# Kernel optimization log

Measured on AMD Instinct MI355X. Metric: run time of the kernel, lower is better.

## Reference

```python
import jax, jax.numpy as jnp
import numpy as np

B, T, S, D = 8, 2048, 2048, 1024

def setup_inputs() -> dict:
    key = jax.random.key(0)
    k1, k2 = jax.random.split(key)
    trg_outs = jax.random.normal(k1, (B, T, D), dtype=jnp.float32)
    src_outs = jax.random.normal(k2, (B, S, D), dtype=jnp.float32)
    return {"trg_outs": trg_outs, "src_outs": src_outs}

def reference(trg_outs, src_outs):
    # Luong 'dot' attention: unscaled dot-product scores.
    # scores: (B, T, S)
    attn_scores = jnp.einsum('btd,bsd->bts', trg_outs, src_outs)
    attn_weights = jax.nn.softmax(attn_scores, axis=2)
    # context: (B, T, D)
    context_vec = jnp.einsum('bts,bsd->btd', attn_weights, src_outs)
    return (context_vec, attn_weights)
```

## Files before the change

### kernel.cpp

```cpp
#include <hip/hip_runtime.h>


#define BB 8
#define TT 2048
#define SS 2048
#define DD 1024

typedef float  f32x4   __attribute__((ext_vector_type(4)));
typedef float  f32x16  __attribute__((ext_vector_type(16)));
typedef short  bf16x8  __attribute__((ext_vector_type(8)));
typedef _Float16 f16x8 __attribute__((ext_vector_type(8)));
typedef _Float16 f16x4 __attribute__((ext_vector_type(4)));

static __device__ __forceinline__ unsigned short bf16_rne(float x) {
  unsigned int u = __float_as_uint(x);
  u += 0x7FFFu + ((u >> 16) & 1u);
  return (unsigned short)(u >> 16);
}

static __device__ __forceinline__ void gl2lds16(const void* g, void* l) {
  __builtin_amdgcn_global_load_lds(
      (const __attribute__((address_space(1))) unsigned int*)g,
      (__attribute__((address_space(3))) unsigned int*)l, 16, 0, 0);
}

__global__ __launch_bounds__(256)
void conv_trg_f16(const float* __restrict__ x, _Float16* __restrict__ h16) {
  const size_t i = ((size_t)blockIdx.x * 256 + threadIdx.x) * 8;
  float4 v0 = *(const float4*)(x + i);
  float4 v1 = *(const float4*)(x + i + 4);
  f16x8 h;
  h[0] = (_Float16)v0.x; h[1] = (_Float16)v0.y;
  h[2] = (_Float16)v0.z; h[3] = (_Float16)v0.w;
  h[4] = (_Float16)v1.x; h[5] = (_Float16)v1.y;
  h[6] = (_Float16)v1.z; h[7] = (_Float16)v1.w;
  *(f16x8*)(h16 + i) = h;
}

__global__ __launch_bounds__(256)
void conv_src_f16_hilo_t(const float* __restrict__ src,
                         _Float16* __restrict__ hi,
                         _Float16* __restrict__ lo,
                         _Float16* __restrict__ srcT) {
  const int b  = blockIdx.z;
  const int d0 = blockIdx.x * 64;
  const int s0 = blockIdx.y * 64;
  const float* S = src + (size_t)b * SS * DD;
  __shared__ _Float16 t16[64][65];
  const int t = threadIdx.x;

#pragma unroll
  for (int p = 0; p < 4; ++p) {
    const int r = p * 16 + (t >> 4);
    const int c = (t & 15) * 4;
    float4 v = *(const float4*)(S + (size_t)(s0 + r) * DD + d0 + c);
    float f[4] = {v.x, v.y, v.z, v.w};
    f16x4 h, l;
#pragma unroll
    for (int e = 0; e < 4; ++e) {
      _Float16 hv = (_Float16)f[e];
      h[e] = hv;
      l[e] = (_Float16)(f[e] - (float)hv);
      t16[r][c + e] = hv;
    }
    const size_t go = ((size_t)b * SS + s0 + r) * DD + d0 + c;
    *(f16x4*)(hi + go) = h;
    *(f16x4*)(lo + go) = l;
  }
  __syncthreads();
#pragma unroll
  for (int p = 0; p < 4; ++p) {
    const int d  = p * 16 + (t >> 4);
    const int sq = (t & 15) * 4;
    f16x4 o;
#pragma unroll
    for (int k = 0; k < 4; ++k) o[k] = t16[sq + k][d];
    *(f16x4*)(srcT + ((size_t)b * DD + d0 + d) * SS + s0 + sq) = o;
  }
}

__global__ __launch_bounds__(512, 2)
void attn_gemm1_pipe(const _Float16* __restrict__ a16,
                     const _Float16* __restrict__ bh16,
                     const _Float16* __restrict__ bl16,
                     float* __restrict__ scores) {
  const int b   = blockIdx.z;
  const int tm0 = blockIdx.y * 256;
  const int tn0 = blockIdx.x * 256;
  float* C = scores + (size_t)b * TT * SS;

  __shared__ __align__(16) _Float16 sm[3][3][8192];

  const int t      = threadIdx.x;
  const int lane   = t & 63;
  const int wv     = t >> 6;
  const int wm     = (wv >> 2) * 128;
  const int wn     = (wv & 3) * 64;
  const int lrow32 = lane & 31;
  const int khalf  = lane >> 5;

  const int s0 = t, s1 = t + 512;
  const int r0 = s0 >> 2, g0 = (s0 & 3) ^ ((r0 >> 1) & 3);
  const int r1 = s1 >> 2, g1 = (s1 & 3) ^ ((r1 >> 1) & 3);

  const _Float16* pA0  = a16  + ((size_t)b * TT + tm0 + r0) * DD + g0 * 8;
  const _Float16* pA1  = a16  + ((size_t)b * TT + tm0 + r1) * DD + g1 * 8;
  const _Float16* pBh0 = bh16 + ((size_t)b * SS + tn0 + r0) * DD + g0 * 8;
  const _Float16* pBh1 = bh16 + ((size_t)b * SS + tn0 + r1) * DD + g1 * 8;
  const _Float16* pBl0 = bl16 + ((size_t)b * SS + tn0 + r0) * DD + g0 * 8;
  const _Float16* pBl1 = bl16 + ((size_t)b * SS + tn0 + r1) * DD + g1 * 8;

#define STAGE1(dst)                                    \
  do {                                                 \
    gl2lds16(pA0,  (dst) + s0 * 8);                    \
    gl2lds16(pA1,  (dst) + s1 * 8);                    \
    gl2lds16(pBh0, (dst) + 8192 + s0 * 8);             \
    gl2lds16(pBh1, (dst) + 8192 + s1 * 8);             \
    gl2lds16(pBl0, (dst) + 16384 + s0 * 8);            \
    gl2lds16(pBl1, (dst) + 16384 + s1 * 8);            \
    pA0 += 32; pA1 += 32; pBh0 += 32; pBh1 += 32;      \
    pBl0 += 32; pBl1 += 32;                            \
  } while (0)

  f32x16 acc[4][2];
#pragma unroll
  for (int i = 0; i < 4; ++i)
#pragma unroll
    for (int j = 0; j < 2; ++j) acc[i][j] = (f32x16)0.0f;

  _Float16* bufc = &sm[0][0][0];
  _Float16* bufo = &sm[1][0][0];
  _Float16* bufn = &sm[2][0][0];

  STAGE1(bufc);
  STAGE1(bufo);
  asm volatile("s_waitcnt vmcnt(6)" ::: "memory");
  __builtin_amdgcn_s_barrier();
  __builtin_amdgcn_sched_barrier(0);

  const int NT = DD / 32;
#pragma unroll 1
  for (int tt = 0; tt < NT; ++tt) {
    if (tt + 2 < NT) STAGE1(bufn);

    const _Float16* As = bufc;
    const _Float16* Bh = bufc + 8192;
    const _Float16* Bl = bufc + 16384;
#pragma unroll
    for (int kk = 0; kk < 2; ++kk) {
      const int cb = kk * 2 + khalf;
      f16x8 a[4], bh[2], bl[2];
#pragma unroll
      for (int mi = 0; mi < 4; ++mi) {
        const int r = wm + mi * 32 + lrow32;
        a[mi] = *(const f16x8*)(As + (r * 4 + (cb ^ ((r >> 1) & 3))) * 8);
      }
#pragma unroll
      for (int ni = 0; ni < 2; ++ni) {
        const int r   = wn + ni * 32 + lrow32;
        const int off = (r * 4 + (cb ^ ((r >> 1) & 3))) * 8;
        bh[ni] = *(const f16x8*)(Bh + off);
        bl[ni] = *(const f16x8*)(Bl + off);
      }
      __builtin_amdgcn_s_setprio(1);
#pragma unroll
      for (int mi = 0; mi < 4; ++mi)
#pragma unroll
        for (int ni = 0; ni < 2; ++ni) {
          acc[mi][ni] = __builtin_amdgcn_mfma_f32_32x32x16_f16(a[mi], bh[ni], acc[mi][ni], 0, 0, 0);
          acc[mi][ni] = __builtin_amdgcn_mfma_f32_32x32x16_f16(a[mi], bl[ni], acc[mi][ni], 0, 0, 0);
        }
      __builtin_amdgcn_s_setprio(0);
    }

    if (tt + 2 < NT) asm volatile("s_waitcnt vmcnt(6)" ::: "memory");
    else             asm volatile("s_waitcnt vmcnt(0)" ::: "memory");
    __builtin_amdgcn_s_barrier();
    __builtin_amdgcn_sched_barrier(0);

    _Float16* tmp = bufc; bufc = bufo; bufo = bufn; bufn = tmp;
  }
#undef STAGE1

  const int rsub = 4 * khalf;
#pragma unroll
  for (int mi = 0; mi < 4; ++mi)
#pragma unroll
    for (int ni = 0; ni < 2; ++ni) {
      const int rb  = tm0 + wm + mi * 32 + rsub;
      const int col = tn0 + wn + ni * 32 + lrow32;
#pragma unroll
      for (int p = 0; p < 16; ++p)
        C[(size_t)(rb + (p & 3) + 8 * (p >> 2)) * SS + col] = acc[mi][ni][p];
    }
}

__global__ __launch_bounds__(64)
void attn_softmax_w16(float* __restrict__ w, _Float16* __restrict__ w16) {
  const size_t row = blockIdx.x;
  float4* p4 = (float4*)(w + row * SS);
  _Float16* o = w16 + row * SS;
  const int lane = threadIdx.x;

  float4 v[8];
#pragma unroll
  for (int j = 0; j < 8; ++j) v[j] = p4[lane + 64 * j];

  float m = -1e30f;
#pragma unroll
  for (int j = 0; j < 8; ++j)
    m = fmaxf(m, fmaxf(fmaxf(v[j].x, v[j].y), fmaxf(v[j].z, v[j].w)));
#pragma unroll
  for (int off = 32; off >= 1; off >>= 1) m = fmaxf(m, __shfl_xor(m, off, 64));

  float s = 0.0f;
#pragma unroll
  for (int j = 0; j < 8; ++j) {
    v[j].x = __expf(v[j].x - m); v[j].y = __expf(v[j].y - m);
    v[j].z = __expf(v[j].z - m); v[j].w = __expf(v[j].w - m);
    s += v[j].x + v[j].y + v[j].z + v[j].w;
  }
#pragma unroll
  for (int off = 32; off >= 1; off >>= 1) s += __shfl_xor(s, off, 64);

  const float inv = __fdividef(1.0f, s);
#pragma unroll
  for (int j = 0; j < 8; ++j) {
    v[j].x *= inv; v[j].y *= inv; v[j].z *= inv; v[j].w *= inv;
    p4[lane + 64 * j] = v[j];
    f16x4 h;
    h[0] = (_Float16)v[j].x; h[1] = (_Float16)v[j].y;
    h[2] = (_Float16)v[j].z; h[3] = (_Float16)v[j].w;
    *(f16x4*)(o + 4 * (lane + 64 * j)) = h;
  }
}

__global__ __launch_bounds__(512, 2)
void attn_gemm2_pipe(const _Float16* __restrict__ w16,
                     const _Float16* __restrict__ srcT,
                     float* __restrict__ out) {
  const int b   = blockIdx.z;
  const int tm0 = blockIdx.y * 256;
  const int tn0 = blockIdx.x * 256;
  float* C = out + (size_t)b * TT * DD;

  __shared__ __align__(16) _Float16 sm[3][2][8192];

  const int t      = threadIdx.x;
  const int lane   = t & 63;
  const int wv     = t >> 6;
  const int wm     = (wv >> 2) * 128;
  const int wn     = (wv & 3) * 64;
  const int lrow32 = lane & 31;
  const int khalf  = lane >> 5;

  const int s0 = t, s1 = t + 512;
  const int r0 = s0 >> 2, g0 = (s0 & 3) ^ ((r0 >> 1) & 3);
  const int r1 = s1 >> 2, g1 = (s1 & 3) ^ ((r1 >> 1) & 3);

  const _Float16* pA0 = w16  + ((size_t)b * TT + tm0 + r0) * SS + g0 * 8;
  const _Float16* pA1 = w16  + ((size_t)b * TT + tm0 + r1) * SS + g1 * 8;
  const _Float16* pB0 = srcT + ((size_t)b * DD + tn0 + r0) * SS + g0 * 8;
  const _Float16* pB1 = srcT + ((size_t)b * DD + tn0 + r1) * SS + g1 * 8;

#define STAGE2(dst)                                    \
  do {                                                 \
    gl2lds16(pA0, (dst) + s0 * 8);                     \
    gl2lds16(pA1, (dst) + s1 * 8);                     \
    gl2lds16(pB0, (dst) + 8192 + s0 * 8);              \
    gl2lds16(pB1, (dst) + 8192 + s1 * 8);              \
    pA0 += 32; pA1 += 32; pB0 += 32; pB1 += 32;        \
  } while (0)

  f32x16 acc[4][2];
#pragma unroll
  for (int i = 0; i < 4; ++i)
#pragma unroll
    for (int j = 0; j < 2; ++j) acc[i][j] = (f32x16)0.0f;

  _Float16* bufc = &sm[0][0][0];
  _Float16* bufo = &sm[1][0][0];
  _Float16* bufn = &sm[2][0][0];

  STAGE2(bufc);
  STAGE2(bufo);
  asm volatile("s_waitcnt vmcnt(4)" ::: "memory");
  __builtin_amdgcn_s_barrier();
  __builtin_amdgcn_sched_barrier(0);

  const int NT = SS / 32;
#pragma unroll 1
  for (int tt = 0; tt < NT; ++tt) {
    if (tt + 2 < NT) STAGE2(bufn);

    const _Float16* As = bufc;
    const _Float16* Bs = bufc + 8192;
#pragma unroll
    for (int kk = 0; kk < 2; ++kk) {
      const int cb = kk * 2 + khalf;
      f16x8 a[4], bf[2];
#pragma unroll
      for (int mi = 0; mi < 4; ++mi) {
        const int r = wm + mi * 32 + lrow32;
        a[mi] = *(const f16x8*)(As + (r * 4 + (cb ^ ((r >> 1) & 3))) * 8);
      }
#pragma unroll
      for (int ni = 0; ni < 2; ++ni) {
        const int r = wn + ni * 32 + lrow32;
        bf[ni] = *(const f16x8*)(Bs + (r * 4 + (cb ^ ((r >> 1) & 3))) * 8);
      }
      __builtin_amdgcn_s_setprio(1);
#pragma unroll
      for (int mi = 0; mi < 4; ++mi)
#pragma unroll
        for (int ni = 0; ni < 2; ++ni)
          acc[mi][ni] = __builtin_amdgcn_mfma_f32_32x32x16_f16(a[mi], bf[ni], acc[mi][ni], 0, 0, 0);
      __builtin_amdgcn_s_setprio(0);
    }

    if (tt + 2 < NT) asm volatile("s_waitcnt vmcnt(4)" ::: "memory");
    else             asm volatile("s_waitcnt vmcnt(0)" ::: "memory");
    __builtin_amdgcn_s_barrier();
    __builtin_amdgcn_sched_barrier(0);

    _Float16* tmp = bufc; bufc = bufo; bufo = bufn; bufn = tmp;
  }
#undef STAGE2

  const int rsub = 4 * khalf;
#pragma unroll
  for (int mi = 0; mi < 4; ++mi)
#pragma unroll
    for (int ni = 0; ni < 2; ++ni) {
      const int rb  = tm0 + wm + mi * 32 + rsub;
      const int col = tn0 + wn + ni * 32 + lrow32;
#pragma unroll
      for (int p = 0; p < 16; ++p)
        C[(size_t)(rb + (p & 3) + 8 * (p >> 2)) * DD + col] = acc[mi][ni][p];
    }
}

__global__ __launch_bounds__(256, 1)
void attn_gemm1_scores_bf16x3(const float* __restrict__ trg,
                              const float* __restrict__ src,
                              float* __restrict__ scores) {
  const int b   = blockIdx.z;
  const int tm0 = blockIdx.y * 128;
  const int tn0 = blockIdx.x * 128;
  const float* A  = trg + (size_t)b * TT * DD;
  const float* Bm = src + (size_t)b * SS * DD;
  float* C = scores + (size_t)b * TT * SS;

  __shared__ __align__(16) unsigned short smAh[128 * 32];
  __shared__ __align__(16) unsigned short smAl[128 * 32];
  __shared__ __align__(16) unsigned short smBh[128 * 32];
  __shared__ __align__(16) unsigned short smBl[128 * 32];

  const int t     = threadIdx.x;
  const int lane  = t & 63;
  const int wv    = t >> 6;
  const int m_off = (wv & 1) * 64;
  const int n_off = (wv >> 1) * 64;
  const int q     = lane >> 4;
  const int lrow  = lane & 15;

  f32x4 acc[4][4];
#pragma unroll
  for (int i = 0; i < 4; ++i)
#pragma unroll
    for (int j = 0; j < 4; ++j) acc[i][j] = (f32x4)0.0f;

  for (int kt = 0; kt < DD; kt += 32) {
    __syncthreads();
#pragma unroll
    for (int h = 0; h < 2; ++h) {
      const int c  = t + h * 256;
      const int r  = c >> 2;
      const int j  = c & 3;
      const int gk = j ^ ((r >> 1) & 3);
      {
        const float* ga = A + (size_t)(tm0 + r) * DD + kt + gk * 8;
        float4 v0 = *(const float4*)ga;
        float4 v1 = *(const float4*)(ga + 4);
        float f[8] = {v0.x, v0.y, v0.z, v0.w, v1.x, v1.y, v1.z, v1.w};
        bf16x8 hi, lo;
#pragma unroll
        for (int e = 0; e < 8; ++e) {
          unsigned short hb = bf16_rne(f[e]);
          hi[e] = (short)hb;
          float hf = __uint_as_float(((unsigned int)hb) << 16);
          lo[e] = (short)bf16_rne(f[e] - hf);
        }
        *(bf16x8*)(smAh + c * 8) = hi;
        *(bf16x8*)(smAl + c * 8) = lo;
      }
      {
        const float* gb = Bm + (size_t)(tn0 + r) * DD + kt + gk * 8;
        float4 v0 = *(const float4*)gb;
        float4 v1 = *(const float4*)(gb + 4);
        float f[8] = {v0.x, v0.y, v0.z, v0.w, v1.x, v1.y, v1.z, v1.w};
        bf16x8 hi, lo;
#pragma unroll
        for (int e = 0; e < 8; ++e) {
          unsigned short hb = bf16_rne(f[e]);
          hi[e] = (short)hb;
          float hf = __uint_as_float(((unsigned int)hb) << 16);
          lo[e] = (short)bf16_rne(f[e] - hf);
        }
        *(bf16x8*)(smBh + c * 8) = hi;
        *(bf16x8*)(smBl + c * 8) = lo;
      }
    }
    __syncthreads();

    bf16x8 ah[4], al[4], bh[4], bl[4];
#pragma unroll
    for (int mi = 0; mi < 4; ++mi) {
      const int r   = m_off + mi * 16 + lrow;
      const int off = (r * 4 + (q ^ ((r >> 1) & 3))) * 8;
      ah[mi] = *(const bf16x8*)(smAh + off);
      al[mi] = *(const bf16x8*)(smAl + off);
    }
#pragma unroll
    for (int ni = 0; ni < 4; ++ni) {
      const int r   = n_off + ni * 16 + lrow;
      const int off = (r * 4 + (q ^ ((r >> 1) & 3))) * 8;
      bh[ni] = *(const bf16x8*)(smBh + off);
      bl[ni] = *(const bf16x8*)(smBl + off);
    }
#pragma unroll
    for (int mi = 0; mi < 4; ++mi)
#pragma unroll
      for (int ni = 0; ni < 4; ++ni) {
        acc[mi][ni] = __builtin_amdgcn_mfma_f32_16x16x32_bf16(al[mi], bh[ni], acc[mi][ni], 0, 0, 0);
        acc[mi][ni] = __builtin_amdgcn_mfma_f32_16x16x32_bf16(ah[mi], bl[ni], acc[mi][ni], 0, 0, 0);
        acc[mi][ni] = __builtin_amdgcn_mfma_f32_16x16x32_bf16(ah[mi], bh[ni], acc[mi][ni], 0, 0, 0);
      }
  }

#pragma unroll
  for (int mi = 0; mi < 4; ++mi)
#pragma unroll
    for (int ni = 0; ni < 4; ++ni) {
      const int row0 = tm0 + m_off + mi * 16 + q * 4;
      const int col  = tn0 + n_off + ni * 16 + lrow;
#pragma unroll
      for (int p = 0; p < 4; ++p)
        C[(size_t)(row0 + p) * SS + col] = acc[mi][ni][p];
    }
}

__global__ __launch_bounds__(256)
void attn_softmax_rows(float* __restrict__ w) {
  float* p = w + (size_t)blockIdx.x * SS;
  const int t = threadIdx.x;
  float4* p4 = (float4*)p;
  float4 v0 = p4[t];
  float4 v1 = p4[t + 256];

  float m = fmaxf(fmaxf(fmaxf(v0.x, v0.y), fmaxf(v0.z, v0.w)),
                  fmaxf(fmaxf(v1.x, v1.y), fmaxf(v1.z, v1.w)));
#pragma unroll
  for (int off = 32; off >= 1; off >>= 1) m = fmaxf(m, __shfl_xor(m, off, 64));
  __shared__ float redm[4];
  __shared__ float reds[4];
  const int wv = t >> 6, lane = t & 63;
  if (lane == 0) redm[wv] = m;
  __syncthreads();
  m = fmaxf(fmaxf(redm[0], redm[1]), fmaxf(redm[2], redm[3]));

  v0.x = __expf(v0.x - m); v0.y = __expf(v0.y - m);
  v0.z = __expf(v0.z - m); v0.w = __expf(v0.w - m);
  v1.x = __expf(v1.x - m); v1.y = __expf(v1.y - m);
  v1.z = __expf(v1.z - m); v1.w = __expf(v1.w - m);

  float s = v0.x + v0.y + v0.z + v0.w + v1.x + v1.y + v1.z + v1.w;
#pragma unroll
  for (int off = 32; off >= 1; off >>= 1) s += __shfl_xor(s, off, 64);
  if (lane == 0) reds[wv] = s;
  __syncthreads();
  s = reds[0] + reds[1] + reds[2] + reds[3];

  const float inv = __fdividef(1.0f, s);
  v0.x *= inv; v0.y *= inv; v0.z *= inv; v0.w *= inv;
  v1.x *= inv; v1.y *= inv; v1.z *= inv; v1.w *= inv;
  p4[t] = v0;
  p4[t + 256] = v1;
}

__global__ __launch_bounds__(256, 1)
void attn_gemm2_ctx_f16(const float* __restrict__ w,
                        const float* __restrict__ src,
                        float* __restrict__ out) {
  const int b   = blockIdx.z;
  const int tm0 = blockIdx.y * 128;
  const int tn0 = blockIdx.x * 128;
  const float* A  = w + (size_t)b * TT * SS;
  const float* Bs = src + (size_t)b * SS * DD;
  float* C = out + (size_t)b * TT * DD;

  __shared__ __align__(16) _Float16 smA[128 * 32];
  __shared__ __align__(16) _Float16 smB[128 * 32];

  const int t     = threadIdx.x;
  const int lane  = t & 63;
  const int wv    = t >> 6;
  const int m_off = (wv & 1) * 64;
  const int n_off = (wv >> 1) * 64;
  const int q     = lane >> 4;
  const int lrow  = lane & 15;

  const int bn    = t & 127;
  const int bh2   = t >> 7;
  const int bs2   = (bn >> 1) & 3;
  const int slot0 = (2 * bh2) ^ bs2;
  const int slot1 = (2 * bh2 + 1) ^ bs2;

  f32x4 acc[4][4];
#pragma unroll
  for (int i = 0; i < 4; ++i)
#pragma unroll
    for (int j = 0; j < 4; ++j) acc[i][j] = (f32x4)0.0f;

  for (int kt = 0; kt < SS; kt += 32) {
    __syncthreads();
#pragma unroll
    for (int h = 0; h < 2; ++h) {
      const int c  = t + h * 256;
      const int r  = c >> 2;
      const int j  = c & 3;
      const int gk = j ^ ((r >> 1) & 3);
      const float* ga = A + (size_t)(tm0 + r) * SS + kt + gk * 8;
      float4 v0 = *(const float4*)ga;
      float4 v1 = *(const float4*)(ga + 4);
      f16x8 hv;
      hv[0] = (_Float16)v0.x; hv[1] = (_Float16)v0.y;
      hv[2] = (_Float16)v0.z; hv[3] = (_Float16)v0.w;
      hv[4] = (_Float16)v1.x; hv[5] = (_Float16)v1.y;
      hv[6] = (_Float16)v1.z; hv[7] = (_Float16)v1.w;
      *(f16x8*)(smA + c * 8) = hv;
    }
    {
      const float* gb = Bs + (size_t)(kt + bh2 * 16) * DD + (tn0 + bn);
      f16x8 c0, c1;
#pragma unroll
      for (int kk = 0; kk < 8; ++kk) c0[kk] = (_Float16)gb[(size_t)kk * DD];
#pragma unroll
      for (int kk = 0; kk < 8; ++kk) c1[kk] = (_Float16)gb[(size_t)(kk + 8) * DD];
      *(f16x8*)(smB + bn * 32 + slot0 * 8) = c0;
      *(f16x8*)(smB + bn * 32 + slot1 * 8) = c1;
    }
    __syncthreads();

    f16x8 af[4], bfr[4];
#pragma unroll
    for (int mi = 0; mi < 4; ++mi) {
      const int r   = m_off + mi * 16 + lrow;
      const int off = (r * 4 + (q ^ ((r >> 1) & 3))) * 8;
      af[mi] = *(const f16x8*)(smA + off);
    }
#pragma unroll
    for (int ni = 0; ni < 4; ++ni) {
      const int n   = n_off + ni * 16 + lrow;
      const int off = n * 32 + (q ^ ((n >> 1) & 3)) * 8;
      bfr[ni] = *(const f16x8*)(smB + off);
    }
#pragma unroll
    for (int mi = 0; mi < 4; ++mi)
#pragma unroll
      for (int ni = 0; ni < 4; ++ni)
        acc[mi][ni] = __builtin_amdgcn_mfma_f32_16x16x32_f16(af[mi], bfr[ni], acc[mi][ni], 0, 0, 0);
  }

#pragma unroll
  for (int mi = 0; mi < 4; ++mi)
#pragma unroll
    for (int ni = 0; ni < 4; ++ni) {
      const int row0 = tm0 + m_off + mi * 16 + q * 4;
      const int col  = tn0 + n_off + ni * 16 + lrow;
#pragma unroll
      for (int p = 0; p < 4; ++p)
        C[(size_t)(row0 + p) * DD + col] = acc[mi][ni][p];
    }
}

extern "C" void kernel_launch(void* const* d_in, const int* in_sizes, int n_in,
                              void* d_out, int out_size, void* d_ws, size_t ws_size,
                              hipStream_t stream) {
  const float* trg = (const float*)d_in[0];
  const float* src = (const float*)d_in[1];
  float* ctx = (float*)d_out;
  float* wts = (float*)d_out + (size_t)BB * TT * DD;

  const size_t NT = (size_t)BB * TT * DD;
  const size_t NW = (size_t)BB * TT * SS;
  const size_t need = (4 * NT + NW) * 2;

  if (ws_size >= need) {
    _Float16* tH16 = (_Float16*)d_ws;
    _Float16* sH16 = tH16 + NT;
    _Float16* sL16 = sH16 + NT;
    _Float16* srcT = sL16 + NT;
    _Float16* w16  = srcT + NT;

    conv_trg_f16<<<dim3(NT / (8 * 256)), 256, 0, stream>>>(trg, tH16);
    conv_src_f16_hilo_t<<<dim3(DD / 64, SS / 64, BB), 256, 0, stream>>>(src, sH16, sL16, srcT);
    attn_gemm1_pipe<<<dim3(SS / 256, TT / 256, BB), 512, 0, stream>>>(tH16, sH16, sL16, wts);
    attn_softmax_w16<<<dim3(BB * TT), 64, 0, stream>>>(wts, w16);
    attn_gemm2_pipe<<<dim3(DD / 256, TT / 256, BB), 512, 0, stream>>>(w16, srcT, ctx);
  } else {
    attn_gemm1_scores_bf16x3<<<dim3(SS / 128, TT / 128, BB), 256, 0, stream>>>(trg, src, wts);
    attn_softmax_rows<<<dim3(BB * TT), 256, 0, stream>>>(wts);
    attn_gemm2_ctx_f16<<<dim3(DD / 128, TT / 128, BB), 256, 0, stream>>>(wts, src, ctx);
  }
}
```

Baseline: 558.6 us.

## Split K-tile into halves with interleaved async loads and barrier ping-pong in GEMMs

Both pipelined GEMM kernels now store each K-tile in LDS as two 16-wide halves, using a new swizzle (ldsoff_h) with LDS offsets computed once outside the loop. Each iteration issues half of the next stage's global-to-LDS loads between the LDS reads and the MFMA block of each half, with extra barriers around the MFMA sections. The goal is to spread memory traffic across the compute phases, reduce per-iteration address arithmetic, and lower LDS bank conflicts. In exchange each iteration has several more barriers, which can stall waves.

```diff
diff --git a/kernel.cpp b/kernel.cpp
--- a/kernel.cpp
+++ b/kernel.cpp
@@ -22,6 +22,10 @@
   __builtin_amdgcn_global_load_lds(
       (const __attribute__((address_space(1))) unsigned int*)g,
       (__attribute__((address_space(3))) unsigned int*)l, 16, 0, 0);
+}
+
+static __device__ __forceinline__ int ldsoff_h(int r, int h) {
+  return ((r >> 2) << 6) + ((((r & 3) << 1) + (h ^ ((r >> 2) & 1))) << 3);
 }
 
 __global__ __launch_bounds__(256)
@@ -89,7 +93,7 @@
   const int tn0 = blockIdx.x * 256;
   float* C = scores + (size_t)b * TT * SS;
 
-  __shared__ __align__(16) _Float16 sm[3][3][8192];
+  __shared__ __align__(16) _Float16 sm[3][24576];
 
   const int t      = threadIdx.x;
   const int lane   = t & 63;
@@ -99,28 +103,34 @@
   const int lrow32 = lane & 31;
   const int khalf  = lane >> 5;
 
-  const int s0 = t, s1 = t + 512;
-  const int r0 = s0 >> 2, g0 = (s0 & 3) ^ ((r0 >> 1) & 3);
-  const int r1 = s1 >> 2, g1 = (s1 & 3) ^ ((r1 >> 1) & 3);
-
-  const _Float16* pA0  = a16  + ((size_t)b * TT + tm0 + r0) * DD + g0 * 8;
-  const _Float16* pA1  = a16  + ((size_t)b * TT + tm0 + r1) * DD + g1 * 8;
-  const _Float16* pBh0 = bh16 + ((size_t)b * SS + tn0 + r0) * DD + g0 * 8;
-  const _Float16* pBh1 = bh16 + ((size_t)b * SS + tn0 + r1) * DD + g1 * 8;
-  const _Float16* pBl0 = bl16 + ((size_t)b * SS + tn0 + r0) * DD + g0 * 8;
-  const _Float16* pBl1 = bl16 + ((size_t)b * SS + tn0 + r1) * DD + g1 * 8;
-
-#define STAGE1(dst)                                    \
-  do {                                                 \
-    gl2lds16(pA0,  (dst) + s0 * 8);                    \
-    gl2lds16(pA1,  (dst) + s1 * 8);                    \
-    gl2lds16(pBh0, (dst) + 8192 + s0 * 8);             \
-    gl2lds16(pBh1, (dst) + 8192 + s1 * 8);             \
-    gl2lds16(pBl0, (dst) + 16384 + s0 * 8);            \
-    gl2lds16(pBl1, (dst) + 16384 + s1 * 8);            \
-    pA0 += 32; pA1 += 32; pBh0 += 32; pBh1 += 32;      \
-    pBl0 += 32; pBl1 += 32;                            \
-  } while (0)
+  const _Float16* gp[6];
+  {
+    const _Float16* base0 = a16  + ((size_t)b * TT + tm0) * DD;
+    const _Float16* base1 = bh16 + ((size_t)b * SS + tn0) * DD;
+    const _Float16* base2 = bl16 + ((size_t)b * SS + tn0) * DD;
+    const _Float16* bases[3] = {base0, base1, base2};
+#pragma unroll
+    for (int j = 0; j < 6; ++j) {
+      const int kk   = j & 1;
+      const int cc   = t;
+      const int line = cc >> 3, slot = cc & 7;
+      const int r    = (line << 2) + (slot >> 1);
+      const int h    = (slot & 1) ^ (line & 1);
+      gp[j] = bases[j >> 1] + (size_t)r * DD + kk * 16 + h * 8;
+    }
+  }
+#define STG1(buf, j) do { gl2lds16(gp[j], (buf) + ((j) * 512 + t) * 8); gp[j] += 32; } while (0)
+
+  int aoff[4], bhoff[2], bloff[2];
+#pragma unroll
+  for (int mi = 0; mi < 4; ++mi)
+    aoff[mi] = ldsoff_h(wm + mi * 32 + lrow32, khalf);
+#pragma unroll
+  for (int ni = 0; ni < 2; ++ni) {
+    const int rr = wn + ni * 32 + lrow32;
+    bhoff[ni] = 8192  + ldsoff_h(rr, khalf);
+    bloff[ni] = 16384 + ldsoff_h(rr, khalf);
+  }
 
   f32x16 acc[4][2];
 #pragma unroll
@@ -128,12 +138,14 @@
 #pragma unroll
     for (int j = 0; j < 2; ++j) acc[i][j] = (f32x16)0.0f;
 
-  _Float16* bufc = &sm[0][0][0];
-  _Float16* bufo = &sm[1][0][0];
-  _Float16* bufn = &sm[2][0][0];
-
-  STAGE1(bufc);
-  STAGE1(bufo);
+  _Float16* bufc = sm[0];
+  _Float16* bufo = sm[1];
+  _Float16* bufn = sm[2];
+
+#pragma unroll
+  for (int j = 0; j < 6; ++j) STG1(bufc, j);
+#pragma unroll
+  for (int j = 0; j < 6; ++j) STG1(bufo, j);
   asm volatile("s_waitcnt vmcnt(6)" ::: "memory");
   __builtin_amdgcn_s_barrier();
   __builtin_amdgcn_sched_barrier(0);
@@ -141,27 +153,21 @@
   const int NT = DD / 32;
 #pragma unroll 1
   for (int tt = 0; tt < NT; ++tt) {
-    if (tt + 2 < NT) STAGE1(bufn);
-
-    const _Float16* As = bufc;
-    const _Float16* Bh = bufc + 8192;
-    const _Float16* Bl = bufc + 16384;
-#pragma unroll
-    for (int kk = 0; kk < 2; ++kk) {
-      const int cb = kk * 2 + khalf;
+    const bool more = (tt + 2 < NT);
+
+    {
       f16x8 a[4], bh[2], bl[2];
 #pragma unroll
-      for (int mi = 0; mi < 4; ++mi) {
-        const int r = wm + mi * 32 + lrow32;
-        a[mi] = *(const f16x8*)(As + (r * 4 + (cb ^ ((r >> 1) & 3))) * 8);
+      for (int mi = 0; mi < 4; ++mi) a[mi] = *(const f16x8*)(bufc + aoff[mi]);
+#pragma unroll
+      for (int ni = 0; ni < 2; ++ni) {
+        bh[ni] = *(const f16x8*)(bufc + bhoff[ni]);
+        bl[ni] = *(const f16x8*)(bufc + bloff[ni]);
       }
-#pragma unroll
-      for (int ni = 0; ni < 2; ++ni) {
-        const int r   = wn + ni * 32 + lrow32;
-        const int off = (r * 4 + (cb ^ ((r >> 1) & 3))) * 8;
-        bh[ni] = *(const f16x8*)(Bh + off);
-        bl[ni] = *(const f16x8*)(Bl + off);
-      }
+      if (more) { STG1(bufn, 0); STG1(bufn, 1); STG1(bufn, 2); }
+      __builtin_amdgcn_s_barrier();
+      asm volatile("s_waitcnt lgkmcnt(0)" ::: "memory");
+      __builtin_amdgcn_sched_barrier(0);
       __builtin_amdgcn_s_setprio(1);
 #pragma unroll
       for (int mi = 0; mi < 4; ++mi)
@@ -171,16 +177,41 @@
           acc[mi][ni] = __builtin_amdgcn_mfma_f32_32x32x16_f16(a[mi], bl[ni], acc[mi][ni], 0, 0, 0);
         }
       __builtin_amdgcn_s_setprio(0);
-    }
-
-    if (tt + 2 < NT) asm volatile("s_waitcnt vmcnt(6)" ::: "memory");
-    else             asm volatile("s_waitcnt vmcnt(0)" ::: "memory");
-    __builtin_amdgcn_s_barrier();
-    __builtin_amdgcn_sched_barrier(0);
+      __builtin_amdgcn_s_barrier();
+      __builtin_amdgcn_sched_barrier(0);
+    }
+
+    {
+      f16x8 a[4], bh[2], bl[2];
+#pragma unroll
+      for (int mi = 0; mi < 4; ++mi) a[mi] = *(const f16x8*)(bufc + 4096 + aoff[mi]);
+#pragma unroll
+      for (int ni = 0; ni < 2; ++ni) {
+        bh[ni] = *(const f16x8*)(bufc + 4096 + bhoff[ni]);
+        bl[ni] = *(const f16x8*)(bufc + 4096 + bloff[ni]);
+      }
+      if (more) { STG1(bufn, 3); STG1(bufn, 4); STG1(bufn, 5); }
+      if (more) asm volatile("s_waitcnt vmcnt(6)" ::: "memory");
+      else      asm volatile("s_waitcnt vmcnt(0)" ::: "memory");
+      __builtin_amdgcn_s_barrier();
+      asm volatile("s_waitcnt lgkmcnt(0)" ::: "memory");
+      __builtin_amdgcn_sched_barrier(0);
+      __builtin_amdgcn_s_setprio(1);
+#pragma unroll
+      for (int mi = 0; mi < 4; ++mi)
+#pragma unroll
+        for (int ni = 0; ni < 2; ++ni) {
+          acc[mi][ni] = __builtin_amdgcn_mfma_f32_32x32x16_f16(a[mi], bh[ni], acc[mi][ni], 0, 0, 0);
+          acc[mi][ni] = __builtin_amdgcn_mfma_f32_32x32x16_f16(a[mi], bl[ni], acc[mi][ni], 0, 0, 0);
+        }
+      __builtin_amdgcn_s_setprio(0);
+      __builtin_amdgcn_s_barrier();
+      __builtin_amdgcn_sched_barrier(0);
+    }
 
     _Float16* tmp = bufc; bufc = bufo; bufo = bufn; bufn = tmp;
   }
-#undef STAGE1
+#undef STG1
 
   const int rsub = 4 * khalf;
 #pragma unroll
@@ -244,7 +275,7 @@
   const int tn0 = blockIdx.x * 256;
   float* C = out + (size_t)b * TT * DD;
 
-  __shared__ __align__(16) _Float16 sm[3][2][8192];
+  __shared__ __align__(16) _Float16 sm[3][16384];
 
   const int t      = threadIdx.x;
   const int lane   = t & 63;
@@ -254,23 +285,30 @@
   const int lrow32 = lane & 31;
   const int khalf  = lane >> 5;
 
-  const int s0 = t, s1 = t + 512;
-  const int r0 = s0 >> 2, g0 = (s0 & 3) ^ ((r0 >> 1) & 3);
-  const int r1 = s1 >> 2, g1 = (s1 & 3) ^ ((r1 >> 1) & 3);
-
-  const _Float16* pA0 = w16  + ((size_t)b * TT + tm0 + r0) * SS + g0 * 8;
-  const _Float16* pA1 = w16  + ((size_t)b * TT + tm0 + r1) * SS + g1 * 8;
-  const _Float16* pB0 = srcT + ((size_t)b * DD + tn0 + r0) * SS + g0 * 8;
-  const _Float16* pB1 = srcT + ((size_t)b * DD + tn0 + r1) * SS + g1 * 8;
-
-#define STAGE2(dst)                                    \
-  do {                                                 \
-    gl2lds16(pA0, (dst) + s0 * 8);                     \
-    gl2lds16(pA1, (dst) + s1 * 8);                     \
-    gl2lds16(pB0, (dst) + 8192 + s0 * 8);              \
-    gl2lds16(pB1, (dst) + 8192 + s1 * 8);              \
-    pA0 += 32; pA1 += 32; pB0 += 32; pB1 += 32;        \
-  } while (0)
+  const _Float16* gp[4];
+  {
+    const _Float16* base0 = w16  + ((size_t)b * TT + tm0) * SS;
+    const _Float16* base1 = srcT + ((size_t)b * DD + tn0) * SS;
+    const _Float16* bases[2] = {base0, base1};
+#pragma unroll
+    for (int j = 0; j < 4; ++j) {
+      const int kk   = j & 1;
+      const int cc   = t;
+      const int line = cc >> 3, slot = cc & 7;
+      const int r    = (line << 2) + (slot >> 1);
+      const int h    = (slot & 1) ^ (line & 1);
+      gp[j] = bases[j >> 1] + (size_t)r * SS + kk * 16 + h * 8;
+    }
+  }
+#define STG2(buf, j) do { gl2lds16(gp[j], (buf) + ((j) * 512 + t) * 8); gp[j] += 32; } while (0)
+
+  int aoff[4], boff[2];
+#pragma unroll
+  for (int mi = 0; mi < 4; ++mi)
+    aoff[mi] = ldsoff_h(wm + mi * 32 + lrow32, khalf);
+#pragma unroll
+  for (int ni = 0; ni < 2; ++ni)
+    boff[ni] = 8192 + ldsoff_h(wn + ni * 32 + lrow32, khalf);
 
   f32x16 acc[4][2];
 #pragma unroll
@@ -278,12 +316,14 @@
 #pragma unroll
     for (int j = 0; j < 2; ++j) acc[i][j] = (f32x16)0.0f;
 
-  _Float16* bufc = &sm[0][0][0];
-  _Float16* bufo = &sm[1][0][0];
-  _Float16* bufn = &sm[2][0][0];
-
-  STAGE2(bufc);
-  STAGE2(bufo);
+  _Float16* bufc = sm[0];
+  _Float16* bufo = sm[1];
+  _Float16* bufn = sm[2];
+
+#pragma unroll
+  for (int j = 0; j < 4; ++j) STG2(bufc, j);
+#pragma unroll
+  for (int j = 0; j < 4; ++j) STG2(bufo, j);
   asm volatile("s_waitcnt vmcnt(4)" ::: "memory");
   __builtin_amdgcn_s_barrier();
   __builtin_amdgcn_sched_barrier(0);
@@ -291,24 +331,18 @@
   const int NT = SS / 32;
 #pragma unroll 1
   for (int tt = 0; tt < NT; ++tt) {
-    if (tt + 2 < NT) STAGE2(bufn);
-
-    const _Float16* As = bufc;
-    const _Float16* Bs = bufc + 8192;
-#pragma unroll
-    for (int kk = 0; kk < 2; ++kk) {
-      const int cb = kk * 2 + khalf;
+    const bool more = (tt + 2 < NT);
+
+    {
       f16x8 a[4], bf[2];
 #pragma unroll
-      for (int mi = 0; mi < 4; ++mi) {
-        const int r = wm + mi * 32 + lrow32;
-        a[mi] = *(const f16x8*)(As + (r * 4 + (cb ^ ((r >> 1) & 3))) * 8);
-      }
-#pragma unroll
-      for (int ni = 0; ni < 2; ++ni) {
-        const int r = wn + ni * 32 + lrow32;
-        bf[ni] = *(const f16x8*)(Bs + (r * 4 + (cb ^ ((r >> 1) & 3))) * 8);
-      }
+      for (int mi = 0; mi < 4; ++mi) a[mi] = *(const f16x8*)(bufc + aoff[mi]);
+#pragma unroll
+      for (int ni = 0; ni < 2; ++ni) bf[ni] = *(const f16x8*)(bufc + boff[ni]);
+      if (more) { STG2(bufn, 0); STG2(bufn, 2); }
+      __builtin_amdgcn_s_barrier();
+      asm volatile("s_waitcnt lgkmcnt(0)" ::: "memory");
+      __builtin_amdgcn_sched_barrier(0);
       __builtin_amdgcn_s_setprio(1);
 #pragma unroll
       for (int mi = 0; mi < 4; ++mi)
@@ -316,16 +350,36 @@
         for (int ni = 0; ni < 2; ++ni)
           acc[mi][ni] = __builtin_amdgcn_mfma_f32_32x32x16_f16(a[mi], bf[ni], acc[mi][ni], 0, 0, 0);
       __builtin_amdgcn_s_setprio(0);
-    }
-
-    if (tt + 2 < NT) asm volatile("s_waitcnt vmcnt(4)" ::: "memory");
-    else             asm volatile("s_waitcnt vmcnt(0)" ::: "memory");
-    __builtin_amdgcn_s_barrier();
-    __builtin_amdgcn_sched_barrier(0);
+      __builtin_amdgcn_s_barrier();
+      __builtin_amdgcn_sched_barrier(0);
+    }
+
+    {
+      f16x8 a[4], bf[2];
+#pragma unroll
+      for (int mi = 0; mi < 4; ++mi) a[mi] = *(const f16x8*)(bufc + 4096 + aoff[mi]);
+#pragma unroll
+      for (int ni = 0; ni < 2; ++ni) bf[ni] = *(const f16x8*)(bufc + 4096 + boff[ni]);
+      if (more) { STG2(bufn, 1); STG2(bufn, 3); }
+      if (more) asm volatile("s_waitcnt vmcnt(4)" ::: "memory");
+      else      asm volatile("s_waitcnt vmcnt(0)" ::: "memory");
+      __builtin_amdgcn_s_barrier();
+      asm volatile("s_waitcnt lgkmcnt(0)" ::: "memory");
+      __builtin_amdgcn_sched_barrier(0);
+      __builtin_amdgcn_s_setprio(1);
+#pragma unroll
+      for (int mi = 0; mi < 4; ++mi)
+#pragma unroll
+        for (int ni = 0; ni < 2; ++ni)
+          acc[mi][ni] = __builtin_amdgcn_mfma_f32_32x32x16_f16(a[mi], bf[ni], acc[mi][ni], 0, 0, 0);
+      __builtin_amdgcn_s_setprio(0);
+      __builtin_amdgcn_s_barrier();
+      __builtin_amdgcn_sched_barrier(0);
+    }
 
     _Float16* tmp = bufc; bufc = bufo; bufo = bufn; bufn = tmp;
   }
-#undef STAGE2
+#undef STG2
 
   const int rsub = 4 * khalf;
 #pragma unroll
```

After: 575.5 us. 1.03x slower.

## Pre-swizzle B operands into MFMA fragment layout and load directly to registers

Applied to the files above, without the earlier changes.

The source conversion kernel now writes the hi/lo f16 split and the transposed copy in a fragment-major layout matching the MFMA 32x32x16 B operand. Both GEMMs then load B fragments straight from global memory into registers, double-buffered across half-k phases, and stage only the A tile through LDS with a new swizzle. This cuts LDS footprint and LDS traffic and removes the B LDS reads. The cost is more global loads per wave (B is no longer shared across waves in the block via LDS), an extra barrier per phase, and hand-tuned vmcnt counts that must match the load order exactly.

```diff
diff --git a/kernel.cpp b/kernel.cpp
--- a/kernel.cpp
+++ b/kernel.cpp
@@ -22,6 +22,10 @@
   __builtin_amdgcn_global_load_lds(
       (const __attribute__((address_space(1))) unsigned int*)g,
       (__attribute__((address_space(3))) unsigned int*)l, 16, 0, 0);
+}
+
+static __device__ __forceinline__ int ldsoff_h(int r, int h) {
+  return ((r >> 2) << 6) + ((((r & 3) << 1) + (h ^ ((r >> 2) & 1))) << 3);
 }
 
 __global__ __launch_bounds__(256)
@@ -38,10 +42,10 @@
 }
 
 __global__ __launch_bounds__(256)
-void conv_src_f16_hilo_t(const float* __restrict__ src,
-                         _Float16* __restrict__ hi,
-                         _Float16* __restrict__ lo,
-                         _Float16* __restrict__ srcT) {
+void conv_src_frag(const float* __restrict__ src,
+                   _Float16* __restrict__ bhp,
+                   _Float16* __restrict__ blp,
+                   _Float16* __restrict__ tp) {
   const int b  = blockIdx.z;
   const int d0 = blockIdx.x * 64;
   const int s0 = blockIdx.y * 64;
@@ -50,46 +54,58 @@
   const int t = threadIdx.x;
 
 #pragma unroll
-  for (int p = 0; p < 4; ++p) {
-    const int r = p * 16 + (t >> 4);
-    const int c = (t & 15) * 4;
-    float4 v = *(const float4*)(S + (size_t)(s0 + r) * DD + d0 + c);
-    float f[4] = {v.x, v.y, v.z, v.w};
-    f16x4 h, l;
-#pragma unroll
-    for (int e = 0; e < 4; ++e) {
+  for (int p = 0; p < 2; ++p) {
+    const int idx  = p * 256 + t;
+    const int dgrp = idx & 7;
+    const int srow = idx >> 3;
+    const float* g = S + (size_t)(s0 + srow) * DD + d0 + dgrp * 8;
+    float4 v0 = *(const float4*)g;
+    float4 v1 = *(const float4*)(g + 4);
+    float f[8] = {v0.x, v0.y, v0.z, v0.w, v1.x, v1.y, v1.z, v1.w};
+    f16x8 h, l;
+#pragma unroll
+    for (int e = 0; e < 8; ++e) {
       _Float16 hv = (_Float16)f[e];
       h[e] = hv;
       l[e] = (_Float16)(f[e] - (float)hv);
-      t16[r][c + e] = hv;
-    }
-    const size_t go = ((size_t)b * SS + s0 + r) * DD + d0 + c;
-    *(f16x4*)(hi + go) = h;
-    *(f16x4*)(lo + go) = l;
+      t16[srow][dgrp * 8 + e] = hv;
+    }
+    const int d   = d0 + dgrp * 8;
+    const int s   = s0 + srow;
+    const size_t base = ((size_t)b * 64 + (d >> 4)) * 32768 +
+                        (size_t)(s >> 5) * 512 +
+                        (size_t)((((d >> 3) & 1) * 32 + (s & 31)) * 8);
+    *(f16x8*)(bhp + base) = h;
+    *(f16x8*)(blp + base) = l;
   }
   __syncthreads();
 #pragma unroll
-  for (int p = 0; p < 4; ++p) {
-    const int d  = p * 16 + (t >> 4);
-    const int sq = (t & 15) * 4;
-    f16x4 o;
-#pragma unroll
-    for (int k = 0; k < 4; ++k) o[k] = t16[sq + k][d];
-    *(f16x4*)(srcT + ((size_t)b * DD + d0 + d) * SS + s0 + sq) = o;
+  for (int p = 0; p < 2; ++p) {
+    const int d64  = t & 63;
+    const int sgrp = p * 4 + (t >> 6);
+    f16x8 o;
+#pragma unroll
+    for (int k = 0; k < 8; ++k) o[k] = t16[sgrp * 8 + k][d64];
+    const int d = d0 + d64;
+    const int s = s0 + sgrp * 8;
+    const size_t base = ((size_t)b * 128 + (s >> 4)) * 16384 +
+                        (size_t)(d >> 5) * 512 +
+                        (size_t)((((s >> 3) & 1) * 32 + (d & 31)) * 8);
+    *(f16x8*)(tp + base) = o;
   }
 }
 
 __global__ __launch_bounds__(512, 2)
 void attn_gemm1_pipe(const _Float16* __restrict__ a16,
-                     const _Float16* __restrict__ bh16,
-                     const _Float16* __restrict__ bl16,
+                     const _Float16* __restrict__ bhp,
+                     const _Float16* __restrict__ blp,
                      float* __restrict__ scores) {
   const int b   = blockIdx.z;
   const int tm0 = blockIdx.y * 256;
   const int tn0 = blockIdx.x * 256;
   float* C = scores + (size_t)b * TT * SS;
 
-  __shared__ __align__(16) _Float16 sm[3][3][8192];
+  __shared__ __align__(16) _Float16 sm[3][8192];
 
   const int t      = threadIdx.x;
   const int lane   = t & 63;
@@ -99,88 +115,96 @@
   const int lrow32 = lane & 31;
   const int khalf  = lane >> 5;
 
-  const int s0 = t, s1 = t + 512;
-  const int r0 = s0 >> 2, g0 = (s0 & 3) ^ ((r0 >> 1) & 3);
-  const int r1 = s1 >> 2, g1 = (s1 & 3) ^ ((r1 >> 1) & 3);
-
-  const _Float16* pA0  = a16  + ((size_t)b * TT + tm0 + r0) * DD + g0 * 8;
-  const _Float16* pA1  = a16  + ((size_t)b * TT + tm0 + r1) * DD + g1 * 8;
-  const _Float16* pBh0 = bh16 + ((size_t)b * SS + tn0 + r0) * DD + g0 * 8;
-  const _Float16* pBh1 = bh16 + ((size_t)b * SS + tn0 + r1) * DD + g1 * 8;
-  const _Float16* pBl0 = bl16 + ((size_t)b * SS + tn0 + r0) * DD + g0 * 8;
-  const _Float16* pBl1 = bl16 + ((size_t)b * SS + tn0 + r1) * DD + g1 * 8;
-
-#define STAGE1(dst)                                    \
-  do {                                                 \
-    gl2lds16(pA0,  (dst) + s0 * 8);                    \
-    gl2lds16(pA1,  (dst) + s1 * 8);                    \
-    gl2lds16(pBh0, (dst) + 8192 + s0 * 8);             \
-    gl2lds16(pBh1, (dst) + 8192 + s1 * 8);             \
-    gl2lds16(pBl0, (dst) + 16384 + s0 * 8);            \
-    gl2lds16(pBl1, (dst) + 16384 + s1 * 8);            \
-    pA0 += 32; pA1 += 32; pBh0 += 32; pBh1 += 32;      \
-    pBl0 += 32; pBl1 += 32;                            \
+  const int ar = (t >> 3) * 4 + ((t & 7) >> 1);
+  const int ah = ((t & 7) & 1) ^ ((t >> 3) & 1);
+  const _Float16* gpA0 = a16 + ((size_t)b * TT + tm0 + ar) * DD + ah * 8;
+  const _Float16* gpA1 = gpA0 + 16;
+
+  const _Float16* bh_base = bhp + (size_t)b * 2097152 +
+                            (size_t)((tn0 + wn) >> 5) * 512 + (size_t)lane * 8;
+  const _Float16* bl_base = blp + (size_t)b * 2097152 +
+                            (size_t)((tn0 + wn) >> 5) * 512 + (size_t)lane * 8;
+
+  int aoff[4];
+#pragma unroll
+  for (int mi = 0; mi < 4; ++mi)
+    aoff[mi] = ldsoff_h(wm + mi * 32 + lrow32, khalf);
+
+  f32x16 acc[4][2];
+#pragma unroll
+  for (int i = 0; i < 4; ++i)
+#pragma unroll
+    for (int j = 0; j < 2; ++j) acc[i][j] = (f32x16)0.0f;
+
+  f16x8 bhA[2], blA[2], bhB[2], blB[2];
+
+  _Float16* bufc = sm[0];
+  _Float16* bufo = sm[1];
+  _Float16* bufn = sm[2];
+
+#define G1_LOADB(QQ, BH, BL)                                                \
+  do {                                                                      \
+    BH[0] = *(const f16x8*)(bh_base + (size_t)(QQ) * 32768);                \
+    BH[1] = *(const f16x8*)(bh_base + (size_t)(QQ) * 32768 + 512);          \
+    BL[0] = *(const f16x8*)(bl_base + (size_t)(QQ) * 32768);                \
+    BL[1] = *(const f16x8*)(bl_base + (size_t)(QQ) * 32768 + 512);          \
   } while (0)
 
-  f32x16 acc[4][2];
-#pragma unroll
-  for (int i = 0; i < 4; ++i)
-#pragma unroll
-    for (int j = 0; j < 2; ++j) acc[i][j] = (f32x16)0.0f;
-
-  _Float16* bufc = &sm[0][0][0];
-  _Float16* bufo = &sm[1][0][0];
-  _Float16* bufn = &sm[2][0][0];
-
-  STAGE1(bufc);
-  STAGE1(bufo);
-  asm volatile("s_waitcnt vmcnt(6)" ::: "memory");
+#define G1_PHASE(AOFFADD, DOLOADB, QN, BHN, BLN, DOSTAGE, AJ, VM, BHC, BLC) \
+  {                                                                         \
+    f16x8 af[4];                                                            \
+    _Pragma("unroll") for (int mi = 0; mi < 4; ++mi)                        \
+      af[mi] = *(const f16x8*)(bufc + (AOFFADD) + aoff[mi]);                \
+    asm volatile("" ::: "memory");                                          \
+    if (DOLOADB) { G1_LOADB(QN, BHN, BLN); }                                \
+    asm volatile("" ::: "memory");                                          \
+    if (DOSTAGE) {                                                          \
+      gl2lds16((AJ) ? (const void*)gpA1 : (const void*)gpA0,                \
+               bufn + (AJ) * 4096 + t * 8);                                 \
+    }                                                                       \
+    asm volatile("s_waitcnt vmcnt(" #VM ")" ::: "memory");                  \
+    __builtin_amdgcn_s_barrier();                                           \
+    asm volatile("s_waitcnt lgkmcnt(0)" ::: "memory");                      \
+    __builtin_amdgcn_sched_barrier(0);                                      \
+    __builtin_amdgcn_s_setprio(1);                                          \
+    _Pragma("unroll") for (int mi = 0; mi < 4; ++mi)                        \
+      _Pragma("unroll") for (int ni = 0; ni < 2; ++ni) {                    \
+        acc[mi][ni] = __builtin_amdgcn_mfma_f32_32x32x16_f16(af[mi], BHC[ni], acc[mi][ni], 0, 0, 0); \
+        acc[mi][ni] = __builtin_amdgcn_mfma_f32_32x32x16_f16(af[mi], BLC[ni], acc[mi][ni], 0, 0, 0); \
+      }                                                                     \
+    __builtin_amdgcn_s_setprio(0);                                          \
+    __builtin_amdgcn_s_barrier();                                           \
+    __builtin_amdgcn_sched_barrier(0);                                      \
+  }
+
+  gl2lds16(gpA0, sm[0] + t * 8);
+  gl2lds16(gpA1, sm[0] + 4096 + t * 8);
+  gpA0 += 32; gpA1 += 32;
+  asm volatile("" ::: "memory");
+  G1_LOADB(0, bhA, blA);
+  asm volatile("" ::: "memory");
+  gl2lds16(gpA0, sm[1] + t * 8);
+  gl2lds16(gpA1, sm[1] + 4096 + t * 8);
+  gpA0 += 32; gpA1 += 32;
+  asm volatile("s_waitcnt vmcnt(2)" ::: "memory");
   __builtin_amdgcn_s_barrier();
   __builtin_amdgcn_sched_barrier(0);
 
-  const int NT = DD / 32;
 #pragma unroll 1
-  for (int tt = 0; tt < NT; ++tt) {
-    if (tt + 2 < NT) STAGE1(bufn);
-
-    const _Float16* As = bufc;
-    const _Float16* Bh = bufc + 8192;
-    const _Float16* Bl = bufc + 16384;
-#pragma unroll
-    for (int kk = 0; kk < 2; ++kk) {
-      const int cb = kk * 2 + khalf;
-      f16x8 a[4], bh[2], bl[2];
-#pragma unroll
-      for (int mi = 0; mi < 4; ++mi) {
-        const int r = wm + mi * 32 + lrow32;
-        a[mi] = *(const f16x8*)(As + (r * 4 + (cb ^ ((r >> 1) & 3))) * 8);
-      }
-#pragma unroll
-      for (int ni = 0; ni < 2; ++ni) {
-        const int r   = wn + ni * 32 + lrow32;
-        const int off = (r * 4 + (cb ^ ((r >> 1) & 3))) * 8;
-        bh[ni] = *(const f16x8*)(Bh + off);
-        bl[ni] = *(const f16x8*)(Bl + off);
-      }
-      __builtin_amdgcn_s_setprio(1);
-#pragma unroll
-      for (int mi = 0; mi < 4; ++mi)
-#pragma unroll
-        for (int ni = 0; ni < 2; ++ni) {
-          acc[mi][ni] = __builtin_amdgcn_mfma_f32_32x32x16_f16(a[mi], bh[ni], acc[mi][ni], 0, 0, 0);
-          acc[mi][ni] = __builtin_amdgcn_mfma_f32_32x32x16_f16(a[mi], bl[ni], acc[mi][ni], 0, 0, 0);
-        }
-      __builtin_amdgcn_s_setprio(0);
-    }
-
-    if (tt + 2 < NT) asm volatile("s_waitcnt vmcnt(6)" ::: "memory");
-    else             asm volatile("s_waitcnt vmcnt(0)" ::: "memory");
-    __builtin_amdgcn_s_barrier();
-    __builtin_amdgcn_sched_barrier(0);
-
+  for (int tt = 0; tt < 30; ++tt) {
+    G1_PHASE(0,    1, 2 * tt + 1, bhB, blB, 1, 0, 6, bhA, blA);
+    G1_PHASE(4096, 1, 2 * tt + 2, bhA, blA, 1, 1, 6, bhB, blB);
+    gpA0 += 32; gpA1 += 32;
     _Float16* tmp = bufc; bufc = bufo; bufo = bufn; bufn = tmp;
   }
-#undef STAGE1
+  G1_PHASE(0,    1, 61, bhB, blB, 0, 0, 5, bhA, blA);
+  G1_PHASE(4096, 1, 62, bhA, blA, 0, 1, 4, bhB, blB);
+  { _Float16* tmp = bufc; bufc = bufo; bufo = bufn; bufn = tmp; }
+  G1_PHASE(0,    1, 63, bhB, blB, 0, 0, 4, bhA, blA);
+  G1_PHASE(4096, 0, 0,  bhA, blA, 0, 1, 0, bhB, blB);
+
+#undef G1_PHASE
+#undef G1_LOADB
 
   const int rsub = 4 * khalf;
 #pragma unroll
@@ -237,14 +261,14 @@
 
 __global__ __launch_bounds__(512, 2)
 void attn_gemm2_pipe(const _Float16* __restrict__ w16,
-                     const _Float16* __restrict__ srcT,
+                     const _Float16* __restrict__ tp,
                      float* __restrict__ out) {
   const int b   = blockIdx.z;
   const int tm0 = blockIdx.y * 256;
   const int tn0 = blockIdx.x * 256;
   float* C = out + (size_t)b * TT * DD;
 
-  __shared__ __align__(16) _Float16 sm[3][2][8192];
+  __shared__ __align__(16) _Float16 sm[3][8192];
 
   const int t      = threadIdx.x;
   const int lane   = t & 63;
@@ -254,78 +278,90 @@
   const int lrow32 = lane & 31;
   const int khalf  = lane >> 5;
 
-  const int s0 = t, s1 = t + 512;
-  const int r0 = s0 >> 2, g0 = (s0 & 3) ^ ((r0 >> 1) & 3);
-  const int r1 = s1 >> 2, g1 = (s1 & 3) ^ ((r1 >> 1) & 3);
-
-  const _Float16* pA0 = w16  + ((size_t)b * TT + tm0 + r0) * SS + g0 * 8;
-  const _Float16* pA1 = w16  + ((size_t)b * TT + tm0 + r1) * SS + g1 * 8;
-  const _Float16* pB0 = srcT + ((size_t)b * DD + tn0 + r0) * SS + g0 * 8;
-  const _Float16* pB1 = srcT + ((size_t)b * DD + tn0 + r1) * SS + g1 * 8;
-
-#define STAGE2(dst)                                    \
-  do {                                                 \
-    gl2lds16(pA0, (dst) + s0 * 8);                     \
-    gl2lds16(pA1, (dst) + s1 * 8);                     \
-    gl2lds16(pB0, (dst) + 8192 + s0 * 8);              \
-    gl2lds16(pB1, (dst) + 8192 + s1 * 8);              \
-    pA0 += 32; pA1 += 32; pB0 += 32; pB1 += 32;        \
+  const int ar = (t >> 3) * 4 + ((t & 7) >> 1);
+  const int ah = ((t & 7) & 1) ^ ((t >> 3) & 1);
+  const _Float16* gpA0 = w16 + ((size_t)b * TT + tm0 + ar) * SS + ah * 8;
+  const _Float16* gpA1 = gpA0 + 16;
+
+  const _Float16* tb_base = tp + (size_t)b * 2097152 +
+                            (size_t)((tn0 + wn) >> 5) * 512 + (size_t)lane * 8;
+
+  int aoff[4];
+#pragma unroll
+  for (int mi = 0; mi < 4; ++mi)
+    aoff[mi] = ldsoff_h(wm + mi * 32 + lrow32, khalf);
+
+  f32x16 acc[4][2];
+#pragma unroll
+  for (int i = 0; i < 4; ++i)
+#pragma unroll
+    for (int j = 0; j < 2; ++j) acc[i][j] = (f32x16)0.0f;
+
+  f16x8 bfA[2], bfB[2];
+
+  _Float16* bufc = sm[0];
+  _Float16* bufo = sm[1];
+  _Float16* bufn = sm[2];
+
+#define G2_LOADB(QQ, BF)                                                    \
+  do {                                                                      \
+    BF[0] = *(const f16x8*)(tb_base + (size_t)(QQ) * 16384);                \
+    BF[1] = *(const f16x8*)(tb_base + (size_t)(QQ) * 16384 + 512);          \
   } while (0)
 
-  f32x16 acc[4][2];
-#pragma unroll
-  for (int i = 0; i < 4; ++i)
-#pragma unroll
-    for (int j = 0; j < 2; ++j) acc[i][j] = (f32x16)0.0f;
-
-  _Float16* bufc = &sm[0][0][0];
-  _Float16* bufo = &sm[1][0][0];
-  _Float16* bufn = &sm[2][0][0];
-
-  STAGE2(bufc);
-  STAGE2(bufo);
-  asm volatile("s_waitcnt vmcnt(4)" ::: "memory");
+#define G2_PHASE(AOFFADD, DOLOADB, QN, BFN, DOSTAGE, AJ, VM, BFC)           \
+  {                                                                         \
+    f16x8 af[4];                                                            \
+    _Pragma("unroll") for (int mi = 0; mi < 4; ++mi)                        \
+      af[mi] = *(const f16x8*)(bufc + (AOFFADD) + aoff[mi]);                \
+    asm volatile("" ::: "memory");                                          \
+    if (DOLOADB) { G2_LOADB(QN, BFN); }                                     \
+    asm volatile("" ::: "memory");                                          \
+    if (DOSTAGE) {                                                          \
+      gl2lds16((AJ) ? (const void*)gpA1 : (const void*)gpA0,                \
+               bufn + (AJ) * 4096 + t * 8);                                 \
+    }                                                                       \
+    asm volatile("s_waitcnt vmcnt(" #VM ")" ::: "memory");                  \
+    __builtin_amdgcn_s_barrier();                                           \
+    asm volatile("s_waitcnt lgkmcnt(0)" ::: "memory");                      \
+    __builtin_amdgcn_sched_barrier(0);                                      \
+    __builtin_amdgcn_s_setprio(1);                                          \
+    _Pragma("unroll") for (int mi = 0; mi < 4; ++mi)                        \
+      _Pragma("unroll") for (int ni = 0; ni < 2; ++ni)                      \
+        acc[mi][ni] = __builtin_amdgcn_mfma_f32_32x32x16_f16(af[mi], BFC[ni], acc[mi][ni], 0, 0, 0); \
+    __builtin_amdgcn_s_setprio(0);                                          \
+    __builtin_amdgcn_s_barrier();                                           \
+    __builtin_amdgcn_sched_barrier(0);                                      \
+  }
+
+  gl2lds16(gpA0, sm[0] + t * 8);
+  gl2lds16(gpA1, sm[0] + 4096 + t * 8);
+  gpA0 += 32; gpA1 += 32;
+  asm volatile("" ::: "memory");
+  G2_LOADB(0, bfA);
+  asm volatile("" ::: "memory");
+  gl2lds16(gpA0, sm[1] + t * 8);
+  gl2lds16(gpA1, sm[1] + 4096 + t * 8);
+  gpA0 += 32; gpA1 += 32;
+  asm volatile("s_waitcnt vmcnt(2)" ::: "memory");
   __builtin_amdgcn_s_barrier();
   __builtin_amdgcn_sched_barrier(0);
 
-  const int NT = SS / 32;
 #pragma unroll 1
-  for (int tt = 0; tt < NT; ++tt) {
-    if (tt + 2 < NT) STAGE2(bufn);
-
-    const _Float16* As = bufc;
-    const _Float16* Bs = bufc + 8192;
-#pragma unroll
-    for (int kk = 0; kk < 2; ++kk) {
-      const int cb = kk * 2 + khalf;
-      f16x8 a[4], bf[2];
-#pragma unroll
-      for (int mi = 0; mi < 4; ++mi) {
-        const int r = wm + mi * 32 + lrow32;
-        a[mi] = *(const f16x8*)(As + (r * 4 + (cb ^ ((r >> 1) & 3))) * 8);
-      }
-#pragma unroll
-      for (int ni = 0; ni < 2; ++ni) {
-        const int r = wn + ni * 32 + lrow32;
-        bf[ni] = *(const f16x8*)(Bs + (r * 4 + (cb ^ ((r >> 1) & 3))) * 8);
-      }
-      __builtin_amdgcn_s_setprio(1);
-#pragma unroll
-      for (int mi = 0; mi < 4; ++mi)
-#pragma unroll
-        for (int ni = 0; ni < 2; ++ni)
-          acc[mi][ni] = __builtin_amdgcn_mfma_f32_32x32x16_f16(a[mi], bf[ni], acc[mi][ni], 0, 0, 0);
-      __builtin_amdgcn_s_setprio(0);
-    }
-
-    if (tt + 2 < NT) asm volatile("s_waitcnt vmcnt(4)" ::: "memory");
-    else             asm volatile("s_waitcnt vmcnt(0)" ::: "memory");
-    __builtin_amdgcn_s_barrier();
-    __builtin_amdgcn_sched_barrier(0);
-
+  for (int tt = 0; tt < 62; ++tt) {
+    G2_PHASE(0,    1, 2 * tt + 1, bfB, 1, 0, 4, bfA);
+    G2_PHASE(4096, 1, 2 * tt + 2, bfA, 1, 1, 4, bfB);
+    gpA0 += 32; gpA1 += 32;
     _Float16* tmp = bufc; bufc = bufo; bufo = bufn; bufn = tmp;
   }
-#undef STAGE2
+  G2_PHASE(0,    1, 125, bfB, 0, 0, 3, bfA);
+  G2_PHASE(4096, 1, 126, bfA, 0, 1, 2, bfB);
+  { _Float16* tmp = bufc; bufc = bufo; bufo = bufn; bufn = tmp; }
+  G2_PHASE(0,    1, 127, bfB, 0, 0, 2, bfA);
+  G2_PHASE(4096, 0, 0,   bfA, 0, 1, 0, bfB);
+
+#undef G2_PHASE
+#undef G2_LOADB
 
   const int rsub = 4 * khalf;
 #pragma unroll
@@ -598,16 +634,16 @@
 
   if (ws_size >= need) {
     _Float16* tH16 = (_Float16*)d_ws;
-    _Float16* sH16 = tH16 + NT;
-    _Float16* sL16 = sH16 + NT;
-    _Float16* srcT = sL16 + NT;
-    _Float16* w16  = srcT + NT;
+    _Float16* bhp  = tH16 + NT;
+    _Float16* blp  = bhp + NT;
+    _Float16* tp   = blp + NT;
+    _Float16* w16  = tp + NT;
 
     conv_trg_f16<<<dim3(NT / (8 * 256)), 256, 0, stream>>>(trg, tH16);
-    conv_src_f16_hilo_t<<<dim3(DD / 64, SS / 64, BB), 256, 0, stream>>>(src, sH16, sL16, srcT);
-    attn_gemm1_pipe<<<dim3(SS / 256, TT / 256, BB), 512, 0, stream>>>(tH16, sH16, sL16, wts);
+    conv_src_frag<<<dim3(DD / 64, SS / 64, BB), 256, 0, stream>>>(src, bhp, blp, tp);
+    attn_gemm1_pipe<<<dim3(SS / 256, TT / 256, BB), 512, 0, stream>>>(tH16, bhp, blp, wts);
     attn_softmax_w16<<<dim3(BB * TT), 64, 0, stream>>>(wts, w16);
-    attn_gemm2_pipe<<<dim3(DD / 256, TT / 256, BB), 512, 0, stream>>>(w16, srcT, ctx);
+    attn_gemm2_pipe<<<dim3(DD / 256, TT / 256, BB), 512, 0, stream>>>(w16, tp, ctx);
   } else {
     attn_gemm1_scores_bf16x3<<<dim3(SS / 128, TT / 128, BB), 256, 0, stream>>>(trg, src, wts);
     attn_softmax_rows<<<dim3(BB * TT), 256, 0, stream>>>(wts);
```

After: 589.3 us. 1.05x slower.
